# Optimization experiments

Hardware: AMD Instinct MI355X
Metric: run time of the kernel (lower is better)

Reference implementation:

```python
import jax, jax.numpy as jnp
import numpy as np

D, DFFN, H, P, L = 256, 1024, 8, 4, 4
B, LQ = 32, 300
LENS = [2048, 1024, 512, 256]
STARTS = [0, 2048, 3072, 3584]
S = sum(LENS)


def setup_inputs() -> dict:
    key = jax.random.key(0)
    ks = iter(jax.random.split(key, 64))
    def W(shape, s=0.02):
        return jax.random.normal(next(ks), shape, jnp.float32) * s
    inp = {}
    inp['tgt'] = W((B, LQ, D), 1.0)
    inp['query_pos'] = W((B, LQ, D), 1.0)
    centers = jax.random.uniform(next(ks), (B, LQ, L))
    widths = 0.05 + 0.2 * jax.random.uniform(next(ks), (B, LQ, L))
    inp['reference_points'] = jnp.stack([centers, widths], -1)  # (B,Lq,L,2) = (center,width)
    inp['src'] = W((B, S, D), 1.0)
    inp['temporal_lengths'] = np.array(LENS, np.int64)
    inp['level_start_index'] = np.array(STARTS, np.int64)
    for n, shape in [('sa_qw', (D, D)), ('sa_kw', (D, D)), ('sa_vw', (D, D)), ('sa_ow', (D, D)), ('ff1_w', (D, DFFN)), ('ff2_w', (DFFN, D))]:
        inp[n] = W(shape)
    for n, sz in [('sa_qb', D), ('sa_kb', D), ('sa_vb', D), ('sa_ob', D), ('ff1_b', DFFN), ('ff2_b', D)]:
        inp[n] = jnp.zeros((sz,), jnp.float32)
    for pre in ['ca', 'se']:
        inp[pre + '_off_w'] = W((D, H * L * P))
        inp[pre + '_off_b'] = jnp.zeros((H * L * P,), jnp.float32)
        inp[pre + '_attn_w'] = W((D, H * L * P))
        inp[pre + '_attn_b'] = jnp.zeros((H * L * P,), jnp.float32)
        inp[pre + '_val_w'] = W((D, D))
        inp[pre + '_val_b'] = jnp.zeros((D,), jnp.float32)
        inp[pre + '_out_w'] = W((D, D))
        inp[pre + '_out_b'] = jnp.zeros((D,), jnp.float32)
    for n in ['ln1', 'lnse', 'ln2', 'ln3']:
        inp[n + '_g'] = jnp.ones((D,), jnp.float32)
        inp[n + '_b'] = jnp.zeros((D,), jnp.float32)
    return inp


def _ln(x, g, b, eps=1e-5):
    m = jnp.mean(x, -1, keepdims=True)
    v = jnp.mean((x - m) ** 2, -1, keepdims=True)
    return (x - m) * jax.lax.rsqrt(v + eps) * g + b


def _mha(q, k, v, qw, qb, kw, kb, vw, vb, ow, ob):
    b, lq, d = q.shape
    dh = d // H
    qh = (q @ qw + qb).reshape(b, lq, H, dh).transpose(0, 2, 1, 3)
    kh = (k @ kw + kb).reshape(b, -1, H, dh).transpose(0, 2, 1, 3)
    vh = (v @ vw + vb).reshape(b, -1, H, dh).transpose(0, 2, 1, 3)
    scores = jnp.einsum('bhqd,bhkd->bhqk', qh, kh) * (dh ** -0.5)
    attn = jax.nn.softmax(scores, -1)
    out = jnp.einsum('bhqk,bhkd->bhqd', attn, vh).transpose(0, 2, 1, 3).reshape(b, lq, d)
    return out @ ow + ob


def _deform(q, ref, src, lens, starts, vw, vb, offw, offb, aw, ab, ow, ob, boundary):
    b, lq, d = q.shape
    dh = d // H
    value = (src @ vw + vb).reshape(b, -1, H, dh)  # (B,S,H,Dh)
    off = (q @ offw + offb).reshape(b, lq, H, L, P)
    attn = jax.nn.softmax((q @ aw + ab).reshape(b, lq, H, L * P), -1).reshape(b, lq, H, L, P)
    center = ref[..., 0][:, :, None, :, None]  # (B,Lq,1,L,1)
    width = ref[..., 1][:, :, None, :, None]
    if boundary:
        # half the points anchored at segment start, half at segment end
        sign = jnp.where(jnp.arange(P) < P // 2, -0.5, 0.5)
        anchor = center + sign * width
    else:
        anchor = center
    loc = anchor + off / P * width * 0.5  # normalized sampling locations (B,Lq,H,L,P)
    out = jnp.zeros((b, lq, H, dh), value.dtype)
    for l in range(L):
        T = int(lens[l]); s0 = int(starts[l])
        v = value[:, s0:s0 + T].transpose(0, 2, 1, 3)  # (B,H,T,Dh)
        x = loc[:, :, :, l, :] * T - 0.5  # align_corners=False grid
        x0 = jnp.floor(x)
        w = x - x0
        i0 = x0.astype(jnp.int32)
        i1 = i0 + 1
        m0 = ((i0 >= 0) & (i0 < T)).astype(v.dtype)
        m1 = ((i1 >= 0) & (i1 < T)).astype(v.dtype)
        i0c = jnp.clip(i0, 0, T - 1)
        i1c = jnp.clip(i1, 0, T - 1)
        def gather(idx):
            idxh = idx.transpose(0, 2, 1, 3).reshape(b, H, lq * P, 1)
            g = jnp.take_along_axis(v, jnp.broadcast_to(idxh, (b, H, lq * P, dh)), axis=2)
            return g.reshape(b, H, lq, P, dh).transpose(0, 2, 1, 3, 4)  # (B,Lq,H,P,Dh)
        samp = gather(i0c) * ((1 - w) * m0)[..., None] + gather(i1c) * (w * m1)[..., None]
        out = out + jnp.einsum('bqhp,bqhpd->bqhd', attn[:, :, :, l, :], samp)
    return out.reshape(b, lq, d) @ ow + ob


def reference(tgt, query_pos, reference_points, src, temporal_lengths, level_start_index,
              sa_qw, sa_qb, sa_kw, sa_kb, sa_vw, sa_vb, sa_ow, sa_ob,
              ca_off_w, ca_off_b, ca_attn_w, ca_attn_b, ca_val_w, ca_val_b, ca_out_w, ca_out_b,
              se_off_w, se_off_b, se_attn_w, se_attn_b, se_val_w, se_val_b, se_out_w, se_out_b,
              ff1_w, ff1_b, ff2_w, ff2_b,
              ln1_g, ln1_b, lnse_g, lnse_b, ln2_g, ln2_b, ln3_g, ln3_b):
    lens = np.asarray(temporal_lengths)
    starts = np.asarray(level_start_index)
    q = tgt + query_pos
    t2 = _mha(q, q, tgt, sa_qw, sa_qb, sa_kw, sa_kb, sa_vw, sa_vb, sa_ow, sa_ob)
    tgt = _ln(tgt + t2, ln2_g, ln2_b)
    t2 = _deform(tgt + query_pos, reference_points, src, lens, starts,
                 ca_val_w, ca_val_b, ca_off_w, ca_off_b, ca_attn_w, ca_attn_b, ca_out_w, ca_out_b, False)
    tgt = _ln(tgt + t2, ln1_g, ln1_b)
    t2 = _deform(tgt + query_pos, reference_points, src, lens, starts,
                 se_val_w, se_val_b, se_off_w, se_off_b, se_attn_w, se_attn_b, se_out_w, se_out_b, True)
    tgt = _ln(tgt + t2, lnse_g, lnse_b)
    t2 = jax.nn.relu(tgt @ ff1_w + ff1_b) @ ff2_w + ff2_b
    tgt = _ln(tgt + t2, ln3_g, ln3_b)
    return tgt
```

## Files before the change

### kernel.cpp

```cpp
#include <hip/hip_runtime.h>
#include <hip/hip_bf16.h>

namespace {

typedef unsigned short u16;
typedef unsigned int u32;

constexpr int D    = 256;
constexpr int H    = 8;
constexpr int DH   = 32;
constexpr int L    = 4;
constexpr int P    = 4;
constexpr int B    = 32;
constexpr int LQ   = 300;
constexpr int NQ   = B * LQ;
constexpr int S    = 3840;
constexpr int MS   = B * S;
constexpr int DFFN = 1024;

typedef __attribute__((ext_vector_type(8))) short bf16x8;
typedef __attribute__((ext_vector_type(4))) float f32x4;

__device__ inline u16 f2b(float x) {
  u32 u = __builtin_bit_cast(u32, x);
  u32 r = (u + 0x7FFFu + ((u >> 16) & 1u)) >> 16;
  return (u16)r;
}
__device__ inline u32 pk2(float a, float b) {
  return (u32)f2b(a) | ((u32)f2b(b) << 16);
}
__device__ inline void unpack2(u32 w, float& a, float& b) {
  a = __builtin_bit_cast(float, w << 16);
  b = __builtin_bit_cast(float, w & 0xffff0000u);
}

template<bool OUT_BF16, bool RELU>
__global__ __launch_bounds__(256) void gemm_sm(
    const u16* __restrict__ A, const u16* __restrict__ Bt,
    const float* __restrict__ bias, void* __restrict__ Cv,
    int M, int K, int N)
{
  constexpr int BM = 64, BN = 64, BK = 64, LDK = 72;
  __shared__ __align__(16) u16 sh[(BM + BN) * LDK];
  u16* As = sh;
  u16* Bs = sh + BM * LDK;
  const int tid  = threadIdx.x;
  const int lane = tid & 63;
  const int wid  = tid >> 6;
  const int wm = wid >> 1, wn = wid & 1;
  const int m0 = blockIdx.y * BM, n0 = blockIdx.x * BN;

  f32x4 acc[2][2] = {};
  uint4 ra[2], rb[2];
  const int NT = K / BK;
  const int srow = tid >> 3, sch = (tid & 7) * 8;

#pragma unroll
  for (int i = 0; i < 2; ++i) {
    const int row = srow + i * 32;
    ra[i] = *(const uint4*)(A  + (size_t)(m0 + row) * K + sch);
    rb[i] = *(const uint4*)(Bt + (size_t)(n0 + row) * K + sch);
  }

  for (int t = 0; t < NT; ++t) {
#pragma unroll
    for (int i = 0; i < 2; ++i) {
      const int row = srow + i * 32;
      *(uint4*)(&As[row * LDK + sch]) = ra[i];
      *(uint4*)(&Bs[row * LDK + sch]) = rb[i];
    }
    __syncthreads();
    if (t + 1 < NT) {
      const int k0 = (t + 1) * BK;
#pragma unroll
      for (int i = 0; i < 2; ++i) {
        const int row = srow + i * 32;
        ra[i] = *(const uint4*)(A  + (size_t)(m0 + row) * K + k0 + sch);
        rb[i] = *(const uint4*)(Bt + (size_t)(n0 + row) * K + k0 + sch);
      }
    }
#pragma unroll
    for (int kk = 0; kk < 2; ++kk) {
      const int krd = kk * 32 + (lane >> 4) * 8;
      bf16x8 af[2], bf[2];
#pragma unroll
      for (int m = 0; m < 2; ++m)
        af[m] = *(const bf16x8*)(&As[(wm * 32 + (lane & 15) + 16 * m) * LDK + krd]);
#pragma unroll
      for (int n = 0; n < 2; ++n)
        bf[n] = *(const bf16x8*)(&Bs[(wn * 32 + (lane & 15) + 16 * n) * LDK + krd]);
#pragma unroll
      for (int m = 0; m < 2; ++m)
#pragma unroll
        for (int n = 0; n < 2; ++n)
          acc[m][n] = __builtin_amdgcn_mfma_f32_16x16x32_bf16(af[m], bf[n], acc[m][n], 0, 0, 0);
    }
    __syncthreads();
  }

  const int cr = (lane >> 4) * 4;
  const int cc = lane & 15;
  if constexpr (OUT_BF16) {
    u16* stg = sh;
#pragma unroll
    for (int n = 0; n < 2; ++n) {
      const int lc = wn * 32 + n * 16 + cc;
      const float bv = bias[n0 + lc];
#pragma unroll
      for (int m = 0; m < 2; ++m) {
        const int lr0 = wm * 32 + m * 16 + cr;
#pragma unroll
        for (int r = 0; r < 4; ++r) {
          float x = acc[m][n][r] + bv;
          if (RELU) x = fmaxf(x, 0.f);
          stg[(lr0 + r) * LDK + lc] = f2b(x);
        }
      }
    }
    __syncthreads();
    u16* Cb = (u16*)Cv;
#pragma unroll
    for (int i = 0; i < 2; ++i) {
      const int c = tid + 256 * i;
      const int row = c >> 3, ch = c & 7;
      *(uint4*)(Cb + (size_t)(m0 + row) * N + n0 + ch * 8) =
          *(const uint4*)(&stg[row * LDK + ch * 8]);
    }
  } else {
#pragma unroll
    for (int n = 0; n < 2; ++n) {
      const int gc = n0 + wn * 32 + n * 16 + cc;
      const float bv = bias[gc];
#pragma unroll
      for (int m = 0; m < 2; ++m) {
        const int gr0 = m0 + wm * 32 + m * 16 + cr;
#pragma unroll
        for (int r = 0; r < 4; ++r) {
          float x = acc[m][n][r] + bv;
          if (RELU) x = fmaxf(x, 0.f);
          ((float*)Cv)[(size_t)(gr0 + r) * N + gc] = x;
        }
      }
    }
  }
}

__global__ __launch_bounds__(256) void gemm_qkv(
    const u16* __restrict__ qbuf, const u16* __restrict__ tgtb,
    const u16* __restrict__ saqk_t, const u16* __restrict__ sav_t,
    const float* __restrict__ qkb, const float* __restrict__ vbias,
    u16* __restrict__ qkbuf, u16* __restrict__ vh)
{
  constexpr int K = 256, BK = 64, LDK = 72;
  __shared__ __align__(16) u16 sh[128 * LDK];
  u16* As = sh;
  u16* Bs = sh + 64 * LDK;
  const bool isv = blockIdx.x >= 8;
  const u16* A  = isv ? tgtb : qbuf;
  const u16* Bt = isv ? sav_t : saqk_t;
  const float* bias = isv ? vbias : qkb;
  u16* C = isv ? vh : qkbuf;
  const int N = isv ? 256 : 512;
  const int n0 = (isv ? (int)blockIdx.x - 8 : (int)blockIdx.x) * 64;
  const int m0 = blockIdx.y * 64;

  const int tid  = threadIdx.x;
  const int lane = tid & 63;
  const int wid  = tid >> 6;
  const int wm = wid >> 1, wn = wid & 1;

  f32x4 acc[2][2] = {};
  uint4 ra[2], rb[2];
  const int srow = tid >> 3, sch = (tid & 7) * 8;

#pragma unroll
  for (int i = 0; i < 2; ++i) {
    const int row = srow + i * 32;
    ra[i] = *(const uint4*)(A  + (size_t)(m0 + row) * K + sch);
    rb[i] = *(const uint4*)(Bt + (size_t)(n0 + row) * K + sch);
  }
  for (int t = 0; t < 4; ++t) {
#pragma unroll
    for (int i = 0; i < 2; ++i) {
      const int row = srow + i * 32;
      *(uint4*)(&As[row * LDK + sch]) = ra[i];
      *(uint4*)(&Bs[row * LDK + sch]) = rb[i];
    }
    __syncthreads();
    if (t + 1 < 4) {
      const int k0 = (t + 1) * BK;
#pragma unroll
      for (int i = 0; i < 2; ++i) {
        const int row = srow + i * 32;
        ra[i] = *(const uint4*)(A  + (size_t)(m0 + row) * K + k0 + sch);
        rb[i] = *(const uint4*)(Bt + (size_t)(n0 + row) * K + k0 + sch);
      }
    }
#pragma unroll
    for (int kk = 0; kk < 2; ++kk) {
      const int krd = kk * 32 + (lane >> 4) * 8;
      bf16x8 af[2], bf[2];
#pragma unroll
      for (int m = 0; m < 2; ++m)
        af[m] = *(const bf16x8*)(&As[(wm * 32 + (lane & 15) + 16 * m) * LDK + krd]);
#pragma unroll
      for (int n = 0; n < 2; ++n)
        bf[n] = *(const bf16x8*)(&Bs[(wn * 32 + (lane & 15) + 16 * n) * LDK + krd]);
#pragma unroll
      for (int m = 0; m < 2; ++m)
#pragma unroll
        for (int n = 0; n < 2; ++n)
          acc[m][n] = __builtin_amdgcn_mfma_f32_16x16x32_bf16(af[m], bf[n], acc[m][n], 0, 0, 0);
    }
    __syncthreads();
  }

  const int cr = (lane >> 4) * 4;
  const int cc = lane & 15;
  u16* stg = sh;
#pragma unroll
  for (int n = 0; n < 2; ++n) {
    const int lc = wn * 32 + n * 16 + cc;
    const float bv = bias[n0 + lc];
#pragma unroll
    for (int m = 0; m < 2; ++m) {
      const int lr0 = wm * 32 + m * 16 + cr;
#pragma unroll
      for (int r = 0; r < 4; ++r)
        stg[(lr0 + r) * LDK + lc] = f2b(acc[m][n][r] + bv);
    }
  }
  __syncthreads();
#pragma unroll
  for (int i = 0; i < 2; ++i) {
    const int c = tid + 256 * i;
    const int row = c >> 3, ch = c & 7;
    *(uint4*)(C + (size_t)(m0 + row) * N + n0 + ch * 8) =
        *(const uint4*)(&stg[row * LDK + ch * 8]);
  }
}

__global__ __launch_bounds__(512) void gemm_val4(
    const float* __restrict__ A, const u16* __restrict__ Bt2,
    const float* __restrict__ bias2, u16* __restrict__ Vca, u16* __restrict__ Vse)
{
  __shared__ __align__(16) char shraw[33792];
  char* Asw = shraw;
  const int tid  = threadIdx.x;
  const int lane = tid & 63;
  const int w    = tid >> 6;
  const int nh   = blockIdx.x & 1;
  const int m0   = (blockIdx.x >> 1) * 64;
  u16* dst = nh ? Vse : Vca;
  const u16* Bt = Bt2 + nh * 256 * 256;
  const float* bias = bias2 + nh * 256;

#pragma unroll
  for (int i = 0; i < 4; ++i) {
    const int idx = tid + 512 * i;
    const int row = idx >> 5, ch = idx & 31;
    const float* ap = A + (size_t)(m0 + row) * 256 + ch * 8;
    const float4 f0 = *(const float4*)(ap);
    const float4 f1 = *(const float4*)(ap + 4);
    uint4 pk;
    pk.x = pk2(f0.x, f0.y); pk.y = pk2(f0.z, f0.w);
    pk.z = pk2(f1.x, f1.y); pk.w = pk2(f1.z, f1.w);
    *(uint4*)(Asw + row * 512 + ((ch * 16) ^ ((row & 7) << 4))) = pk;
  }
  __syncthreads();

  f32x4 acc[4][2] = {};
  const u16* bb = Bt + (size_t)(w * 32 + (lane & 15)) * 256 + (lane >> 4) * 8;
  bf16x8 bcur[2], bnxt[2];
#pragma unroll
  for (int n = 0; n < 2; ++n) bcur[n] = *(const bf16x8*)(bb + n * 4096);

#pragma unroll
  for (int kk = 0; kk < 8; ++kk) {
    bf16x8 af[4];
    const int kb = kk * 64 + (lane >> 4) * 16;
#pragma unroll
    for (int m = 0; m < 4; ++m) {
      const int row = m * 16 + (lane & 15);
      af[m] = *(const bf16x8*)(Asw + row * 512 + (kb ^ ((row & 7) << 4)));
    }
    if (kk < 7) {
#pragma unroll
      for (int n = 0; n < 2; ++n)
        bnxt[n] = *(const bf16x8*)(bb + n * 4096 + (kk + 1) * 32);
    }
#pragma unroll
    for (int m = 0; m < 4; ++m)
#pragma unroll
      for (int n = 0; n < 2; ++n)
        acc[m][n] = __builtin_amdgcn_mfma_f32_16x16x32_bf16(af[m], bcur[n], acc[m][n], 0, 0, 0);
#pragma unroll
    for (int n = 0; n < 2; ++n) bcur[n] = bnxt[n];
  }
  __syncthreads();

  constexpr int STC = 264;
  u16* stg = (u16*)shraw;
  const int cr = (lane >> 4) * 4;
  const int cc = lane & 15;
#pragma unroll
  for (int n = 0; n < 2; ++n) {
    const int col = w * 32 + n * 16 + cc;
    const float bv = bias[col];
#pragma unroll
    for (int m = 0; m < 4; ++m) {
      const int r0 = m * 16 + cr;
#pragma unroll
      for (int r = 0; r < 4; ++r)
        stg[(r0 + r) * STC + col] = f2b(acc[m][n][r] + bv);
    }
  }
  __syncthreads();
#pragma unroll
  for (int i = 0; i < 4; ++i) {
    const int c = tid + 512 * i;
    const int row = c >> 5, ch = c & 31;
    *(uint4*)(dst + (size_t)(m0 + row) * 256 + ch * 8) =
        *(const uint4*)(&stg[row * STC + ch * 8]);
  }
}

template<int MODE>
__global__ __launch_bounds__(1024) void gemm_ln(
    const u16* __restrict__ A, const u16* __restrict__ Bt,
    const float* __restrict__ bias, const float* __restrict__ res,
    const float* __restrict__ g, const float* __restrict__ be,
    const float* __restrict__ qpos,
    float* __restrict__ fout, u16* __restrict__ bfout, int K)
{
  constexpr int BK = 64, LDK = 72;
  __shared__ __align__(16) float ftile[64 * 264];
  u16* As = (u16*)ftile;
  u16* Bs = As + 64 * LDK;
  const int tid  = threadIdx.x;
  const int lane = tid & 63;
  const int wid  = tid >> 6;
  const int wm = wid >> 2, wn = wid & 3;
  const int m0 = blockIdx.x * 64;

  f32x4 acc[4] = {};
  const int NT = K / BK;
  const bool am = tid < 512;
  const int arow = tid >> 3, ach = (tid & 7) * 8;

  uint4 ra = {};
  uint4 rb[2];
  if (am) ra = *(const uint4*)(A + (size_t)(m0 + arow) * K + ach);
#pragma unroll
  for (int i = 0; i < 2; ++i) {
    const int idx = tid + 1024 * i;
    const int brow = idx >> 3, bch = (idx & 7) * 8;
    rb[i] = *(const uint4*)(Bt + (size_t)brow * K + bch);
  }

  for (int t = 0; t < NT; ++t) {
    if (am) *(uint4*)(&As[arow * LDK + ach]) = ra;
#pragma unroll
    for (int i = 0; i < 2; ++i) {
      const int idx = tid + 1024 * i;
      const int brow = idx >> 3, bch = (idx & 7) * 8;
      *(uint4*)(&Bs[brow * LDK + bch]) = rb[i];
    }
    __syncthreads();
    if (t + 1 < NT) {
      const int k0 = (t + 1) * BK;
      if (am) ra = *(const uint4*)(A + (size_t)(m0 + arow) * K + k0 + ach);
#pragma unroll
      for (int i = 0; i < 2; ++i) {
        const int idx = tid + 1024 * i;
        const int brow = idx >> 3, bch = (idx & 7) * 8;
        rb[i] = *(const uint4*)(Bt + (size_t)brow * K + k0 + bch);
      }
    }
#pragma unroll
    for (int kk = 0; kk < 2; ++kk) {
      const int krd = kk * 32 + (lane >> 4) * 8;
      bf16x8 af, bf[4];
      af = *(const bf16x8*)(&As[(wm * 16 + (lane & 15)) * LDK + krd]);
#pragma unroll
      for (int n = 0; n < 4; ++n)
        bf[n] = *(const bf16x8*)(&Bs[(wn * 64 + n * 16 + (lane & 15)) * LDK + krd]);
#pragma unroll
      for (int n = 0; n < 4; ++n)
        acc[n] = __builtin_amdgcn_mfma_f32_16x16x32_bf16(af, bf[n], acc[n], 0, 0, 0);
    }
    __syncthreads();
  }

  const int cr = (lane >> 4) * 4;
  const int cc = lane & 15;
#pragma unroll
  for (int n = 0; n < 4; ++n) {
    const int col = wn * 64 + n * 16 + cc;
    const float bv = bias[col];
#pragma unroll
    for (int r = 0; r < 4; ++r)
      ftile[(wm * 16 + cr + r) * 264 + col] = acc[n][r] + bv;
  }
  __syncthreads();

  const int row = tid >> 4, s16 = tid & 15;
  const size_t grow = (size_t)(m0 + row) * 256;
  float vv[16];
  float sum = 0.f;
#pragma unroll
  for (int j = 0; j < 4; ++j) {
    const int col = s16 * 4 + j * 64;
    const float4 fv = *(const float4*)(&ftile[row * 264 + col]);
    const float4 rv = *(const float4*)(res + grow + col);
    vv[j * 4 + 0] = fv.x + rv.x; vv[j * 4 + 1] = fv.y + rv.y;
    vv[j * 4 + 2] = fv.z + rv.z; vv[j * 4 + 3] = fv.w + rv.w;
    sum += vv[j * 4 + 0] + vv[j * 4 + 1] + vv[j * 4 + 2] + vv[j * 4 + 3];
  }
  sum += __shfl_xor(sum, 1, 64);
  sum += __shfl_xor(sum, 2, 64);
  sum += __shfl_xor(sum, 4, 64);
  sum += __shfl_xor(sum, 8, 64);
  const float mean = sum * (1.f / 256.f);
  float sq = 0.f;
#pragma unroll
  for (int k = 0; k < 16; ++k) { const float d = vv[k] - mean; sq += d * d; }
  sq += __shfl_xor(sq, 1, 64);
  sq += __shfl_xor(sq, 2, 64);
  sq += __shfl_xor(sq, 4, 64);
  sq += __shfl_xor(sq, 8, 64);
  const float rstd = rsqrtf(sq * (1.f / 256.f) + 1e-5f);

#pragma unroll
  for (int j = 0; j < 4; ++j) {
    const int col = s16 * 4 + j * 64;
    const float4 gv = *(const float4*)(g + col);
    const float4 bv = *(const float4*)(be + col);
    float4 y;
    y.x = (vv[j * 4 + 0] - mean) * rstd * gv.x + bv.x;
    y.y = (vv[j * 4 + 1] - mean) * rstd * gv.y + bv.y;
    y.z = (vv[j * 4 + 2] - mean) * rstd * gv.z + bv.z;
    y.w = (vv[j * 4 + 3] - mean) * rstd * gv.w + bv.w;
    *(float4*)(fout + grow + col) = y;
    if constexpr (MODE == 0) {
      const float4 qv = *(const float4*)(qpos + grow + col);
      uint2 pk;
      pk.x = pk2(y.x + qv.x, y.y + qv.y);
      pk.y = pk2(y.z + qv.z, y.w + qv.w);
      *(uint2*)(bfout + grow + col) = pk;
    } else if constexpr (MODE == 1) {
      uint2 pk;
      pk.x = pk2(y.x, y.y);
      pk.y = pk2(y.z, y.w);
      *(uint2*)(bfout + grow + col) = pk;
    }
  }
}

struct WSpec { const float* w; u16* wt; int K, N, blk0; };
struct WPack { WSpec s[14]; };

struct PrepArgs {
  const float *ca_off_b, *ca_attn_b, *se_off_b, *se_attn_b;
  const float *sa_qb, *sa_kb, *ca_val_b, *se_val_b;
  float *bias4, *qkb, *valb;
  const float *tgt, *qpos;
  u16 *tgtb, *qbuf;
  int n4, nwt;
};

__global__ __launch_bounds__(256) void prep_all(WPack p, PrepArgs a) {
  __shared__ float tile[32][33];
  const int b = blockIdx.x;
  if (b < a.nwt) {
    int i = 0;
#pragma unroll
    for (int j = 1; j < 14; ++j) if (b >= p.s[j].blk0) i = j;
    const float* w = p.s[i].w;
    u16* wt = p.s[i].wt;
    const int K = p.s[i].K, N = p.s[i].N;
    const int lb = b - p.s[i].blk0;
    const int ntN = N >> 5;
    const int tk = lb / ntN, tn = lb - tk * ntN;
    const int r = threadIdx.x >> 5, c = threadIdx.x & 31;
#pragma unroll
    for (int j = 0; j < 4; ++j)
      tile[r + j * 8][c] = w[(size_t)(tk * 32 + r + j * 8) * N + tn * 32 + c];
    __syncthreads();
#pragma unroll
    for (int j = 0; j < 4; ++j)
      wt[(size_t)(tn * 32 + r + j * 8) * K + tk * 32 + c] = f2b(tile[c][r + j * 8]);
  } else if (b == a.nwt) {
#pragma unroll
    for (int u = 0; u < 2; ++u) {
      const int t = threadIdx.x + 256 * u;
      a.bias4[t] = t < 128 ? a.ca_off_b[t] : t < 256 ? a.ca_attn_b[t - 128]
                 : t < 384 ? a.se_off_b[t - 256] : a.se_attn_b[t - 384];
      a.qkb[t]  = t < 256 ? a.sa_qb[t] : a.sa_kb[t - 256];
      a.valb[t] = t < 256 ? a.ca_val_b[t] : a.se_val_b[t - 256];
    }
  } else {
    const int i = (b - a.nwt - 1) * 256 + threadIdx.x;
    if (i < a.n4) {
      const float4 t = ((const float4*)a.tgt)[i];
      const float4 q = ((const float4*)a.qpos)[i];
      uint2 x, y;
      x.x = pk2(t.x, t.y); x.y = pk2(t.z, t.w);
      y.x = pk2(t.x + q.x, t.y + q.y); y.y = pk2(t.z + q.z, t.w + q.w);
      ((uint2*)a.tgtb)[i] = x;
      ((uint2*)a.qbuf)[i] = y;
    }
  }
}

__global__ __launch_bounds__(512) void mha_v2(
    const u16* __restrict__ qk, const u16* __restrict__ vh,
    u16* __restrict__ out)
{
  __shared__ __align__(16) float Ks[8 * 300 * 4];
  __shared__ __align__(16) float Vs[8 * 300 * 4];
  const int bh  = blockIdx.x & 255;
  const int seg = blockIdx.x >> 8;
  const int b = bh >> 3, h = bh & 7;
  const u16* kbase = qk + (size_t)b * LQ * 512 + 256 + h * DH;
  const u16* vbase = vh + (size_t)b * LQ * D + h * DH;
  for (int e = threadIdx.x; e < 300 * 8; e += 512) {
    const int r = e >> 3, j = e & 7;
    float4 f;
    const uint2 kv = *(const uint2*)(kbase + (size_t)r * 512 + j * 4);
    unpack2(kv.x, f.x, f.y);
    unpack2(kv.y, f.z, f.w);
    *(float4*)(&Ks[(j * 300 + r) * 4]) = f;
    const uint2 vv = *(const uint2*)(vbase + (size_t)r * D + j * 4);
    unpack2(vv.x, f.x, f.y);
    unpack2(vv.y, f.z, f.w);
    *(float4*)(&Vs[(j * 300 + r) * 4]) = f;
  }
  __syncthreads();

  const int lane = threadIdx.x & 63;
  const int lq = (threadIdx.x >> 6) * 16 + (lane >> 2);
  const int kc = lane & 3;
  const int q = seg * 128 + lq;
  if (q >= LQ) return;

  const u16* qrow = qk + (size_t)(b * LQ + q) * 512 + h * DH;
  float qv[DH];
#pragma unroll
  for (int c4 = 0; c4 < 4; ++c4) {
    const uint4 u = *(const uint4*)(qrow + c4 * 8);
    unpack2(u.x, qv[c4 * 8 + 0], qv[c4 * 8 + 1]);
    unpack2(u.y, qv[c4 * 8 + 2], qv[c4 * 8 + 3]);
    unpack2(u.z, qv[c4 * 8 + 4], qv[c4 * 8 + 5]);
    unpack2(u.w, qv[c4 * 8 + 6], qv[c4 * 8 + 7]);
  }
#pragma unroll
  for (int d = 0; d < DH; ++d) qv[d] *= 0.17677669529663689f;

  float o[DH] = {};
  float ssum = 0.f;
  const float* kp = &Ks[kc * 75 * 4];
  const float* vp = &Vs[kc * 75 * 4];
  for (int i = 0; i < 75; ++i) {
    float s = 0.f;
#pragma unroll
    for (int j = 0; j < 8; ++j) {
      const float4 kf = *(const float4*)(kp + i * 4 + j * 1200);
      s += qv[j * 4 + 0] * kf.x + qv[j * 4 + 1] * kf.y
         + qv[j * 4 + 2] * kf.z + qv[j * 4 + 3] * kf.w;
    }
    const float p = __expf(s);
    ssum += p;
#pragma unroll
    for (int j = 0; j < 8; ++j) {
      const float4 vf = *(const float4*)(vp + i * 4 + j * 1200);
      o[j * 4 + 0] += p * vf.x; o[j * 4 + 1] += p * vf.y;
      o[j * 4 + 2] += p * vf.z; o[j * 4 + 3] += p * vf.w;
    }
  }

  ssum += __shfl_xor(ssum, 1, 64);
  ssum += __shfl_xor(ssum, 2, 64);
#pragma unroll
  for (int d = 0; d < DH; ++d) {
    o[d] += __shfl_xor(o[d], 1, 64);
    o[d] += __shfl_xor(o[d], 2, 64);
  }
  const float inv = 1.f / ssum;

  u16* orow = out + (size_t)(b * LQ + q) * D + h * DH;
#pragma unroll
  for (int c = 0; c < 4; ++c) {
    if (kc == c) {
      uint4 w;
      w.x = pk2(o[c * 8 + 0] * inv, o[c * 8 + 1] * inv);
      w.y = pk2(o[c * 8 + 2] * inv, o[c * 8 + 3] * inv);
      w.z = pk2(o[c * 8 + 4] * inv, o[c * 8 + 5] * inv);
      w.w = pk2(o[c * 8 + 6] * inv, o[c * 8 + 7] * inv);
      *(uint4*)(orow + c * 8) = w;
    }
  }
}

template<bool BOUNDARY>
__global__ __launch_bounds__(512) void deform_v2(
    const float* __restrict__ oa, const float* __restrict__ ref,
    const u16* __restrict__ value, u16* __restrict__ out)
{
  __shared__ __align__(16) uint4 owt[4][128];
  const int unit = threadIdx.x >> 7;
  const int bq = blockIdx.x * 4 + unit;
  const int b = bq / LQ;
  const int t = threadIdx.x & 127;
  const int h = t >> 4;
  const int l = (t >> 2) & 3;
  const int p = t & 3;

  const float off   = oa[(size_t)bq * 256 + t];
  const float logit = oa[(size_t)bq * 256 + 128 + t];
  const float center = ref[(size_t)bq * 8 + l * 2 + 0];
  const float width  = ref[(size_t)bq * 8 + l * 2 + 1];

  const float e = __expf(logit);
  float ssum = e;
  ssum += __shfl_xor(ssum, 1, 64);
  ssum += __shfl_xor(ssum, 2, 64);
  ssum += __shfl_xor(ssum, 4, 64);
  ssum += __shfl_xor(ssum, 8, 64);
  const float wa = e / ssum;

  const int T  = 2048 >> l;
  const int s0 = 4096 - (4096 >> l);
  float anchor = center;
  if (BOUNDARY) anchor += (p < 2 ? -0.5f : 0.5f) * width;
  const float loc = anchor + off * width * 0.125f;
  const float x = loc * (float)T - 0.5f;
  const float x0 = floorf(x);
  const float w = x - x0;
  const int i0 = (int)x0;
  const int i1 = i0 + 1;
  const float w0 = (i0 >= 0 && i0 < T) ? wa * (1.f - w) : 0.f;
  const float w1 = (i1 >= 0 && i1 < T) ? wa * w : 0.f;
  const int i0c = min(max(i0, 0), T - 1);
  const int i1c = min(max(i1, 0), T - 1);
  uint4 pack;
  pack.x = (u32)((s0 + i0c) * (D * 2) + h * (DH * 2));
  pack.y = __builtin_bit_cast(u32, w0);
  pack.z = (u32)((s0 + i1c) * (D * 2) + h * (DH * 2));
  pack.w = __builtin_bit_cast(u32, w1);
  owt[unit][t] = pack;
  __syncthreads();

  const int g  = t >> 4;
  const int ln = t & 15;
  const char* vb = (const char*)(value + (size_t)b * S * D) + ln * 4;
  float o0 = 0.f, o1 = 0.f;
#pragma unroll
  for (int j = 0; j < 16; ++j) {
    const uint4 ow = owt[unit][g * 16 + j];
    const u32 v0 = *(const u32*)(vb + ow.x);
    const u32 v1 = *(const u32*)(vb + ow.z);
    const float wt0 = __builtin_bit_cast(float, ow.y);
    const float wt1 = __builtin_bit_cast(float, ow.w);
    float a, c;
    unpack2(v0, a, c); o0 += wt0 * a; o1 += wt0 * c;
    unpack2(v1, a, c); o0 += wt1 * a; o1 += wt1 * c;
  }
  const u32 res = pk2(o0, o1);
  *(u32*)(out + (size_t)bq * D + g * DH + ln * 2) = res;
}

}

extern "C" void kernel_launch(void* const* d_in, const int* in_sizes, int n_in,
                              void* d_out, int out_size, void* d_ws, size_t ws_size,
                              hipStream_t stream)
{
  const float* tgt   = (const float*)d_in[0];
  const float* qpos  = (const float*)d_in[1];
  const float* ref   = (const float*)d_in[2];
  const float* src   = (const float*)d_in[3];
  const float* sa_qw = (const float*)d_in[6];
  const float* sa_kw = (const float*)d_in[7];
  const float* sa_vw = (const float*)d_in[8];
  const float* sa_ow = (const float*)d_in[9];
  const float* ff1_w = (const float*)d_in[10];
  const float* ff2_w = (const float*)d_in[11];
  const float* sa_qb = (const float*)d_in[12];
  const float* sa_kb = (const float*)d_in[13];
  const float* sa_vb = (const float*)d_in[14];
  const float* sa_ob = (const float*)d_in[15];
  const float* ff1_b = (const float*)d_in[16];
  const float* ff2_b = (const float*)d_in[17];
  const float* ca_off_w  = (const float*)d_in[18];
  const float* ca_off_b  = (const float*)d_in[19];
  const float* ca_attn_w = (const float*)d_in[20];
  const float* ca_attn_b = (const float*)d_in[21];
  const float* ca_val_w  = (const float*)d_in[22];
  const float* ca_val_b  = (const float*)d_in[23];
  const float* ca_out_w  = (const float*)d_in[24];
  const float* ca_out_b  = (const float*)d_in[25];
  const float* se_off_w  = (const float*)d_in[26];
  const float* se_off_b  = (const float*)d_in[27];
  const float* se_attn_w = (const float*)d_in[28];
  const float* se_attn_b = (const float*)d_in[29];
  const float* se_val_w  = (const float*)d_in[30];
  const float* se_val_b  = (const float*)d_in[31];
  const float* se_out_w  = (const float*)d_in[32];
  const float* se_out_b  = (const float*)d_in[33];
  const float* ln1_g  = (const float*)d_in[34];
  const float* ln1_b  = (const float*)d_in[35];
  const float* lnse_g = (const float*)d_in[36];
  const float* lnse_b = (const float*)d_in[37];
  const float* ln2_g  = (const float*)d_in[38];
  const float* ln2_b  = (const float*)d_in[39];
  const float* ln3_g  = (const float*)d_in[40];
  const float* ln3_b  = (const float*)d_in[41];

  const size_t ND = (size_t)NQ * D;
  const size_t MD = (size_t)MS * D;

  char* base = (char*)d_ws;
  size_t off = 0;
  auto alloc = [&](size_t bytes) -> void* {
    void* p = base + off;
    off += (bytes + 255) & ~(size_t)255;
    return p;
  };
  u16*  Vca  = (u16*)alloc(MD * 2);
  u16*  Vse  = (u16*)alloc(MD * 2);
  u16*  qkbuf = (u16*)alloc((size_t)NQ * 512 * 2);
  u16*  vh   = (u16*)alloc(ND * 2);
  u16*  qbuf = (u16*)alloc(ND * 2);
  u16*  smpb = (u16*)alloc(ND * 2);
  u16*  tgtb = (u16*)alloc(ND * 2);
  u16*  curb = (u16*)alloc(ND * 2);
  float* cur = (float*)alloc(ND * 4);
  float* oabuf = (float*)alloc((size_t)NQ * 256 * 4);
  float* bias4 = (float*)alloc(512 * 4);
  float* qkb   = (float*)alloc(512 * 4);
  float* valb  = (float*)alloc(512 * 4);

  u16* ffh = Vca;

  WPack pk;
  int wi = 0, blk = 0;
  auto addw = [&](const float* w, int K, int N) -> u16* {
    u16* wt = (u16*)alloc((size_t)K * N * 2);
    pk.s[wi].w = w; pk.s[wi].wt = wt; pk.s[wi].K = K; pk.s[wi].N = N; pk.s[wi].blk0 = blk;
    blk += (K / 32) * (N / 32);
    ++wi;
    return wt;
  };
  u16* saq_t = addw(sa_qw, D, D);
  u16* sak_t = addw(sa_kw, D, D);        (void)sak_t;
  u16* sav_t = addw(sa_vw, D, D);
  u16* sao_t = addw(sa_ow, D, D);
  u16* ff1_t = addw(ff1_w, D, DFFN);
  u16* ff2_t = addw(ff2_w, DFFN, D);
  u16* caoff_t = addw(ca_off_w, D, 128);
  u16* caatt_t = addw(ca_attn_w, D, 128);  (void)caatt_t;
  u16* seoff_t = addw(se_off_w, D, 128);
  u16* seatt_t = addw(se_attn_w, D, 128);  (void)seatt_t;
  u16* caval_t = addw(ca_val_w, D, D);
  u16* seval_t = addw(se_val_w, D, D);     (void)seval_t;
  u16* caout_t = addw(ca_out_w, D, D);
  u16* seout_t = addw(se_out_w, D, D);

  const int n4 = (int)(ND / 4);

  PrepArgs pa;
  pa.ca_off_b = ca_off_b; pa.ca_attn_b = ca_attn_b;
  pa.se_off_b = se_off_b; pa.se_attn_b = se_attn_b;
  pa.sa_qb = sa_qb; pa.sa_kb = sa_kb; pa.ca_val_b = ca_val_b; pa.se_val_b = se_val_b;
  pa.bias4 = bias4; pa.qkb = qkb; pa.valb = valb;
  pa.tgt = tgt; pa.qpos = qpos; pa.tgtb = tgtb; pa.qbuf = qbuf;
  pa.n4 = n4; pa.nwt = blk;
  prep_all<<<blk + 1 + 2400, 256, 0, stream>>>(pk, pa);

  gemm_val4<<<(MS / 64) * 2, 512, 0, stream>>>(src, caval_t, valb, Vca, Vse);

  gemm_qkv<<<dim3(12, 150), 256, 0, stream>>>(qbuf, tgtb, saq_t, sav_t, qkb, sa_vb, qkbuf, vh);
  mha_v2<<<B * H * 3, 512, 0, stream>>>(qkbuf, vh, smpb);
  gemm_ln<0><<<NQ / 64, 1024, 0, stream>>>(smpb, sao_t, sa_ob, tgt, ln2_g, ln2_b, qpos, cur, qbuf, D);

  gemm_sm<false, false><<<dim3(4, 150), 256, 0, stream>>>(qbuf, caoff_t, bias4, oabuf, NQ, D, 256);
  deform_v2<false><<<NQ / 4, 512, 0, stream>>>(oabuf, ref, Vca, smpb);
  gemm_ln<0><<<NQ / 64, 1024, 0, stream>>>(smpb, caout_t, ca_out_b, cur, ln1_g, ln1_b, qpos, cur, qbuf, D);

  gemm_sm<false, false><<<dim3(4, 150), 256, 0, stream>>>(qbuf, seoff_t, bias4 + 256, oabuf, NQ, D, 256);
  deform_v2<true><<<NQ / 4, 512, 0, stream>>>(oabuf, ref, Vse, smpb);
  gemm_ln<1><<<NQ / 64, 1024, 0, stream>>>(smpb, seout_t, se_out_b, cur, lnse_g, lnse_b, nullptr, cur, curb, D);

  gemm_sm<true,  true ><<<dim3(16, 150), 256, 0, stream>>>(curb, ff1_t, ff1_b, ffh, NQ, D, DFFN);
  gemm_ln<2><<<NQ / 64, 1024, 0, stream>>>(ffh, ff2_t, ff2_b, cur, ln3_g, ln3_b, nullptr, (float*)d_out, nullptr, DFFN);
}
```

Before: 474.0 us.

## Merge QKV and value GEMMs into one launch, shrink LN-GEMM tiles, widen deform gathers

Three separate changes. First, the self-attention QKV projection and the src value projection now run as one launch, using 128-wide N tiles for QKV, which removes a launch and lets the two GEMMs share the machine. Second, gemm_ln moves from 64-row tiles with 1024 threads to 16-row tiles with 256 threads, giving 600 blocks instead of 150 for better CU occupancy, at the cost of reloading the full weight matrix per block. Third, the deformable gather loads 16-byte vectors per sample instead of 4-byte words and reduces across lanes with shuffles, cutting the number of load instructions in exchange for shuffle work.

```diff
diff --git a/kernel.cpp b/kernel.cpp
--- a/kernel.cpp
+++ b/kernel.cpp
@@ -9,8 +9,6 @@
 constexpr int D    = 256;
 constexpr int H    = 8;
 constexpr int DH   = 32;
-constexpr int L    = 4;
-constexpr int P    = 4;
 constexpr int B    = 32;
 constexpr int LQ   = 300;
 constexpr int NQ   = B * LQ;
@@ -145,246 +143,245 @@
   }
 }
 
-__global__ __launch_bounds__(256) void gemm_qkv(
+__global__ __launch_bounds__(512) void gemm_big(
+    const float* __restrict__ src, const u16* __restrict__ valw_t,
+    const float* __restrict__ valb, u16* __restrict__ Vca, u16* __restrict__ Vse,
     const u16* __restrict__ qbuf, const u16* __restrict__ tgtb,
     const u16* __restrict__ saqk_t, const u16* __restrict__ sav_t,
     const float* __restrict__ qkb, const float* __restrict__ vbias,
     u16* __restrict__ qkbuf, u16* __restrict__ vh)
 {
-  constexpr int K = 256, BK = 64, LDK = 72;
-  __shared__ __align__(16) u16 sh[128 * LDK];
-  u16* As = sh;
-  u16* Bs = sh + 64 * LDK;
-  const bool isv = blockIdx.x >= 8;
-  const u16* A  = isv ? tgtb : qbuf;
-  const u16* Bt = isv ? sav_t : saqk_t;
-  const float* bias = isv ? vbias : qkb;
-  u16* C = isv ? vh : qkbuf;
-  const int N = isv ? 256 : 512;
-  const int n0 = (isv ? (int)blockIdx.x - 8 : (int)blockIdx.x) * 64;
-  const int m0 = blockIdx.y * 64;
-
+  __shared__ __align__(16) char shraw[33792];
   const int tid  = threadIdx.x;
   const int lane = tid & 63;
-  const int wid  = tid >> 6;
-  const int wm = wid >> 1, wn = wid & 1;
-
-  f32x4 acc[2][2] = {};
-  uint4 ra[2], rb[2];
-  const int srow = tid >> 3, sch = (tid & 7) * 8;
-
-#pragma unroll
-  for (int i = 0; i < 2; ++i) {
-    const int row = srow + i * 32;
-    ra[i] = *(const uint4*)(A  + (size_t)(m0 + row) * K + sch);
-    rb[i] = *(const uint4*)(Bt + (size_t)(n0 + row) * K + sch);
-  }
-  for (int t = 0; t < 4; ++t) {
+  const int bx = blockIdx.x;
+
+  if (bx < 900) {
+    constexpr int K = 256, LDK = 72;
+    u16* As = (u16*)shraw;
+    u16* Bs = As + 64 * LDK;
+    const int nt = bx % 6;
+    const int m0 = (bx / 6) * 64;
+    const bool isv = nt >= 4;
+    const int nrel = isv ? nt - 4 : nt;
+    const u16* A  = isv ? tgtb : qbuf;
+    const u16* Bt = (isv ? sav_t : saqk_t) + (size_t)nrel * 128 * 256;
+    const float* bias = (isv ? vbias : qkb) + nrel * 128;
+    u16* C = isv ? vh : qkbuf;
+    const int N = isv ? 256 : 512;
+    const int n0 = nrel * 128;
+
+    const int wid = tid >> 6;
+    const int wm = wid >> 2, wn = wid & 3;
+
+    f32x4 acc[2][2] = {};
+    const int arow = tid >> 3, ach = (tid & 7) * 8;
+    uint4 ra, rb[2];
+    ra = *(const uint4*)(A + (size_t)(m0 + arow) * K + ach);
 #pragma unroll
     for (int i = 0; i < 2; ++i) {
-      const int row = srow + i * 32;
-      *(uint4*)(&As[row * LDK + sch]) = ra[i];
-      *(uint4*)(&Bs[row * LDK + sch]) = rb[i];
-    }
-    __syncthreads();
-    if (t + 1 < 4) {
-      const int k0 = (t + 1) * BK;
+      const int idx = tid + 512 * i;
+      rb[i] = *(const uint4*)(Bt + (size_t)(idx >> 3) * K + (idx & 7) * 8);
+    }
+    for (int t = 0; t < 4; ++t) {
+      *(uint4*)(&As[arow * LDK + ach]) = ra;
 #pragma unroll
       for (int i = 0; i < 2; ++i) {
-        const int row = srow + i * 32;
-        ra[i] = *(const uint4*)(A  + (size_t)(m0 + row) * K + k0 + sch);
-        rb[i] = *(const uint4*)(Bt + (size_t)(n0 + row) * K + k0 + sch);
-      }
-    }
-#pragma unroll
-    for (int kk = 0; kk < 2; ++kk) {
-      const int krd = kk * 32 + (lane >> 4) * 8;
-      bf16x8 af[2], bf[2];
-#pragma unroll
-      for (int m = 0; m < 2; ++m)
-        af[m] = *(const bf16x8*)(&As[(wm * 32 + (lane & 15) + 16 * m) * LDK + krd]);
-#pragma unroll
-      for (int n = 0; n < 2; ++n)
-        bf[n] = *(const bf16x8*)(&Bs[(wn * 32 + (lane & 15) + 16 * n) * LDK + krd]);
-#pragma unroll
-      for (int m = 0; m < 2; ++m)
+        const int idx = tid + 512 * i;
+        *(uint4*)(&Bs[(idx >> 3) * LDK + (idx & 7) * 8]) = rb[i];
+      }
+      __syncthreads();
+      if (t + 1 < 4) {
+        const int k0 = (t + 1) * 64;
+        ra = *(const uint4*)(A + (size_t)(m0 + arow) * K + k0 + ach);
+#pragma unroll
+        for (int i = 0; i < 2; ++i) {
+          const int idx = tid + 512 * i;
+          rb[i] = *(const uint4*)(Bt + (size_t)(idx >> 3) * K + k0 + (idx & 7) * 8);
+        }
+      }
+#pragma unroll
+      for (int kk = 0; kk < 2; ++kk) {
+        const int krd = kk * 32 + (lane >> 4) * 8;
+        bf16x8 af[2], bf[2];
+#pragma unroll
+        for (int m = 0; m < 2; ++m)
+          af[m] = *(const bf16x8*)(&As[(wm * 32 + m * 16 + (lane & 15)) * LDK + krd]);
 #pragma unroll
         for (int n = 0; n < 2; ++n)
-          acc[m][n] = __builtin_amdgcn_mfma_f32_16x16x32_bf16(af[m], bf[n], acc[m][n], 0, 0, 0);
-    }
-    __syncthreads();
-  }
-
-  const int cr = (lane >> 4) * 4;
-  const int cc = lane & 15;
-  u16* stg = sh;
-#pragma unroll
-  for (int n = 0; n < 2; ++n) {
-    const int lc = wn * 32 + n * 16 + cc;
-    const float bv = bias[n0 + lc];
-#pragma unroll
-    for (int m = 0; m < 2; ++m) {
-      const int lr0 = wm * 32 + m * 16 + cr;
-#pragma unroll
-      for (int r = 0; r < 4; ++r)
-        stg[(lr0 + r) * LDK + lc] = f2b(acc[m][n][r] + bv);
-    }
-  }
-  __syncthreads();
-#pragma unroll
-  for (int i = 0; i < 2; ++i) {
-    const int c = tid + 256 * i;
-    const int row = c >> 3, ch = c & 7;
-    *(uint4*)(C + (size_t)(m0 + row) * N + n0 + ch * 8) =
-        *(const uint4*)(&stg[row * LDK + ch * 8]);
-  }
-}
-
-__global__ __launch_bounds__(512) void gemm_val4(
-    const float* __restrict__ A, const u16* __restrict__ Bt2,
-    const float* __restrict__ bias2, u16* __restrict__ Vca, u16* __restrict__ Vse)
-{
-  __shared__ __align__(16) char shraw[33792];
-  char* Asw = shraw;
-  const int tid  = threadIdx.x;
-  const int lane = tid & 63;
-  const int w    = tid >> 6;
-  const int nh   = blockIdx.x & 1;
-  const int m0   = (blockIdx.x >> 1) * 64;
-  u16* dst = nh ? Vse : Vca;
-  const u16* Bt = Bt2 + nh * 256 * 256;
-  const float* bias = bias2 + nh * 256;
-
-#pragma unroll
-  for (int i = 0; i < 4; ++i) {
-    const int idx = tid + 512 * i;
-    const int row = idx >> 5, ch = idx & 31;
-    const float* ap = A + (size_t)(m0 + row) * 256 + ch * 8;
-    const float4 f0 = *(const float4*)(ap);
-    const float4 f1 = *(const float4*)(ap + 4);
-    uint4 pk;
-    pk.x = pk2(f0.x, f0.y); pk.y = pk2(f0.z, f0.w);
-    pk.z = pk2(f1.x, f1.y); pk.w = pk2(f1.z, f1.w);
-    *(uint4*)(Asw + row * 512 + ((ch * 16) ^ ((row & 7) << 4))) = pk;
-  }
-  __syncthreads();
-
-  f32x4 acc[4][2] = {};
-  const u16* bb = Bt + (size_t)(w * 32 + (lane & 15)) * 256 + (lane >> 4) * 8;
-  bf16x8 bcur[2], bnxt[2];
-#pragma unroll
-  for (int n = 0; n < 2; ++n) bcur[n] = *(const bf16x8*)(bb + n * 4096);
-
-#pragma unroll
-  for (int kk = 0; kk < 8; ++kk) {
-    bf16x8 af[4];
-    const int kb = kk * 64 + (lane >> 4) * 16;
-#pragma unroll
-    for (int m = 0; m < 4; ++m) {
-      const int row = m * 16 + (lane & 15);
-      af[m] = *(const bf16x8*)(Asw + row * 512 + (kb ^ ((row & 7) << 4)));
-    }
-    if (kk < 7) {
-#pragma unroll
-      for (int n = 0; n < 2; ++n)
-        bnxt[n] = *(const bf16x8*)(bb + n * 4096 + (kk + 1) * 32);
-    }
-#pragma unroll
-    for (int m = 0; m < 4; ++m)
-#pragma unroll
-      for (int n = 0; n < 2; ++n)
-        acc[m][n] = __builtin_amdgcn_mfma_f32_16x16x32_bf16(af[m], bcur[n], acc[m][n], 0, 0, 0);
-#pragma unroll
-    for (int n = 0; n < 2; ++n) bcur[n] = bnxt[n];
-  }
-  __syncthreads();
-
-  constexpr int STC = 264;
-  u16* stg = (u16*)shraw;
-  const int cr = (lane >> 4) * 4;
-  const int cc = lane & 15;
-#pragma unroll
-  for (int n = 0; n < 2; ++n) {
-    const int col = w * 32 + n * 16 + cc;
-    const float bv = bias[col];
-#pragma unroll
-    for (int m = 0; m < 4; ++m) {
-      const int r0 = m * 16 + cr;
-#pragma unroll
-      for (int r = 0; r < 4; ++r)
-        stg[(r0 + r) * STC + col] = f2b(acc[m][n][r] + bv);
-    }
-  }
-  __syncthreads();
-#pragma unroll
-  for (int i = 0; i < 4; ++i) {
-    const int c = tid + 512 * i;
-    const int row = c >> 5, ch = c & 31;
-    *(uint4*)(dst + (size_t)(m0 + row) * 256 + ch * 8) =
-        *(const uint4*)(&stg[row * STC + ch * 8]);
+          bf[n] = *(const bf16x8*)(&Bs[(wn * 32 + n * 16 + (lane & 15)) * LDK + krd]);
+#pragma unroll
+        for (int m = 0; m < 2; ++m)
+#pragma unroll
+          for (int n = 0; n < 2; ++n)
+            acc[m][n] = __builtin_amdgcn_mfma_f32_16x16x32_bf16(af[m], bf[n], acc[m][n], 0, 0, 0);
+      }
+      __syncthreads();
+    }
+    constexpr int STC = 136;
+    u16* stg = (u16*)shraw;
+    const int cr = (lane >> 4) * 4;
+    const int cc = lane & 15;
+#pragma unroll
+    for (int n = 0; n < 2; ++n) {
+      const int lc = wn * 32 + n * 16 + cc;
+      const float bv = bias[lc];
+#pragma unroll
+      for (int m = 0; m < 2; ++m) {
+        const int lr0 = wm * 32 + m * 16 + cr;
+#pragma unroll
+        for (int r = 0; r < 4; ++r)
+          stg[(lr0 + r) * STC + lc] = f2b(acc[m][n][r] + bv);
+      }
+    }
+    __syncthreads();
+#pragma unroll
+    for (int i = 0; i < 2; ++i) {
+      const int c = tid + 512 * i;
+      const int row = c >> 4, ch = c & 15;
+      *(uint4*)(C + (size_t)(m0 + row) * N + n0 + ch * 8) =
+          *(const uint4*)(&stg[row * STC + ch * 8]);
+    }
+    return;
+  }
+
+  {
+    const int vx = bx - 900;
+    char* Asw = shraw;
+    const int w    = tid >> 6;
+    const int nh   = vx & 1;
+    const int m0   = (vx >> 1) * 64;
+    u16* dst = nh ? Vse : Vca;
+    const u16* Bt = valw_t + nh * 256 * 256;
+    const float* bias = valb + nh * 256;
+
+#pragma unroll
+    for (int i = 0; i < 4; ++i) {
+      const int idx = tid + 512 * i;
+      const int row = idx >> 5, ch = idx & 31;
+      const float* ap = src + (size_t)(m0 + row) * 256 + ch * 8;
+      const float4 f0 = *(const float4*)(ap);
+      const float4 f1 = *(const float4*)(ap + 4);
+      uint4 pk;
+      pk.x = pk2(f0.x, f0.y); pk.y = pk2(f0.z, f0.w);
+      pk.z = pk2(f1.x, f1.y); pk.w = pk2(f1.z, f1.w);
+      *(uint4*)(Asw + row * 512 + ((ch * 16) ^ ((row & 7) << 4))) = pk;
+    }
+    __syncthreads();
+
+    f32x4 acc[4][2] = {};
+    const u16* bb = Bt + (size_t)(w * 32 + (lane & 15)) * 256 + (lane >> 4) * 8;
+    bf16x8 bcur[2], bnxt[2];
+#pragma unroll
+    for (int n = 0; n < 2; ++n) bcur[n] = *(const bf16x8*)(bb + n * 4096);
+
+#pragma unroll
+    for (int kk = 0; kk < 8; ++kk) {
+      bf16x8 af[4];
+      const int kb = kk * 64 + (lane >> 4) * 16;
+#pragma unroll
+      for (int m = 0; m < 4; ++m) {
+        const int row = m * 16 + (lane & 15);
+        af[m] = *(const bf16x8*)(Asw + row * 512 + (kb ^ ((row & 7) << 4)));
+      }
+      if (kk < 7) {
+#pragma unroll
+        for (int n = 0; n < 2; ++n)
+          bnxt[n] = *(const bf16x8*)(bb + n * 4096 + (kk + 1) * 32);
+      }
+#pragma unroll
+      for (int m = 0; m < 4; ++m)
+#pragma unroll
+        for (int n = 0; n < 2; ++n)
+          acc[m][n] = __builtin_amdgcn_mfma_f32_16x16x32_bf16(af[m], bcur[n], acc[m][n], 0, 0, 0);
+#pragma unroll
+      for (int n = 0; n < 2; ++n) bcur[n] = bnxt[n];
+    }
+    __syncthreads();
+
+    constexpr int STC = 264;
+    u16* stg = (u16*)shraw;
+    const int cr = (lane >> 4) * 4;
+    const int cc = lane & 15;
+#pragma unroll
+    for (int n = 0; n < 2; ++n) {
+      const int col = w * 32 + n * 16 + cc;
+      const float bv = bias[col];
+#pragma unroll
+      for (int m = 0; m < 4; ++m) {
+        const int r0 = m * 16 + cr;
+#pragma unroll
+        for (int r = 0; r < 4; ++r)
+          stg[(r0 + r) * STC + col] = f2b(acc[m][n][r] + bv);
+      }
+    }
+    __syncthreads();
+#pragma unroll
+    for (int i = 0; i < 4; ++i) {
+      const int c = tid + 512 * i;
+      const int row = c >> 5, ch = c & 31;
+      *(uint4*)(dst + (size_t)(m0 + row) * 256 + ch * 8) =
+          *(const uint4*)(&stg[row * STC + ch * 8]);
+    }
   }
 }
 
 template<int MODE>
-__global__ __launch_bounds__(1024) void gemm_ln(
+__global__ __launch_bounds__(256) void gemm_ln(
     const u16* __restrict__ A, const u16* __restrict__ Bt,
     const float* __restrict__ bias, const float* __restrict__ res,
     const float* __restrict__ g, const float* __restrict__ be,
     const float* __restrict__ qpos,
     float* __restrict__ fout, u16* __restrict__ bfout, int K)
 {
-  constexpr int BK = 64, LDK = 72;
-  __shared__ __align__(16) float ftile[64 * 264];
-  u16* As = (u16*)ftile;
-  u16* Bs = As + 64 * LDK;
+  constexpr int LDK = 72;
+  __shared__ __align__(16) char shraw[(16 + 256) * LDK * 2];
+  u16* As = (u16*)shraw;
+  u16* Bs = As + 16 * LDK;
+  float* ftile = (float*)shraw;
   const int tid  = threadIdx.x;
   const int lane = tid & 63;
   const int wid  = tid >> 6;
-  const int wm = wid >> 2, wn = wid & 3;
-  const int m0 = blockIdx.x * 64;
+  const int m0 = blockIdx.x * 16;
 
   f32x4 acc[4] = {};
-  const int NT = K / BK;
-  const bool am = tid < 512;
+  const int NT = K / 64;
   const int arow = tid >> 3, ach = (tid & 7) * 8;
 
   uint4 ra = {};
-  uint4 rb[2];
-  if (am) ra = *(const uint4*)(A + (size_t)(m0 + arow) * K + ach);
-#pragma unroll
-  for (int i = 0; i < 2; ++i) {
-    const int idx = tid + 1024 * i;
-    const int brow = idx >> 3, bch = (idx & 7) * 8;
-    rb[i] = *(const uint4*)(Bt + (size_t)brow * K + bch);
+  uint4 rb[8];
+  if (tid < 128) ra = *(const uint4*)(A + (size_t)(m0 + arow) * K + ach);
+#pragma unroll
+  for (int i = 0; i < 8; ++i) {
+    const int idx = tid + 256 * i;
+    rb[i] = *(const uint4*)(Bt + (size_t)(idx >> 3) * K + (idx & 7) * 8);
   }
 
   for (int t = 0; t < NT; ++t) {
-    if (am) *(uint4*)(&As[arow * LDK + ach]) = ra;
-#pragma unroll
-    for (int i = 0; i < 2; ++i) {
-      const int idx = tid + 1024 * i;
-      const int brow = idx >> 3, bch = (idx & 7) * 8;
-      *(uint4*)(&Bs[brow * LDK + bch]) = rb[i];
+    if (tid < 128) *(uint4*)(&As[arow * LDK + ach]) = ra;
+#pragma unroll
+    for (int i = 0; i < 8; ++i) {
+      const int idx = tid + 256 * i;
+      *(uint4*)(&Bs[(idx >> 3) * LDK + (idx & 7) * 8]) = rb[i];
     }
     __syncthreads();
     if (t + 1 < NT) {
-      const int k0 = (t + 1) * BK;
-      if (am) ra = *(const uint4*)(A + (size_t)(m0 + arow) * K + k0 + ach);
-#pragma unroll
-      for (int i = 0; i < 2; ++i) {
-        const int idx = tid + 1024 * i;
-        const int brow = idx >> 3, bch = (idx & 7) * 8;
-        rb[i] = *(const uint4*)(Bt + (size_t)brow * K + k0 + bch);
+      const int k0 = (t + 1) * 64;
+      if (tid < 128) ra = *(const uint4*)(A + (size_t)(m0 + arow) * K + k0 + ach);
+#pragma unroll
+      for (int i = 0; i < 8; ++i) {
+        const int idx = tid + 256 * i;
+        rb[i] = *(const uint4*)(Bt + (size_t)(idx >> 3) * K + k0 + (idx & 7) * 8);
       }
     }
 #pragma unroll
     for (int kk = 0; kk < 2; ++kk) {
       const int krd = kk * 32 + (lane >> 4) * 8;
       bf16x8 af, bf[4];
-      af = *(const bf16x8*)(&As[(wm * 16 + (lane & 15)) * LDK + krd]);
+      af = *(const bf16x8*)(&As[(lane & 15) * LDK + krd]);
 #pragma unroll
       for (int n = 0; n < 4; ++n)
-        bf[n] = *(const bf16x8*)(&Bs[(wn * 64 + n * 16 + (lane & 15)) * LDK + krd]);
+        bf[n] = *(const bf16x8*)(&Bs[(wid * 64 + n * 16 + (lane & 15)) * LDK + krd]);
 #pragma unroll
       for (int n = 0; n < 4; ++n)
         acc[n] = __builtin_amdgcn_mfma_f32_16x16x32_bf16(af, bf[n], acc[n], 0, 0, 0);
@@ -396,11 +393,11 @@
   const int cc = lane & 15;
 #pragma unroll
   for (int n = 0; n < 4; ++n) {
-    const int col = wn * 64 + n * 16 + cc;
+    const int col = wid * 64 + n * 16 + cc;
     const float bv = bias[col];
 #pragma unroll
     for (int r = 0; r < 4; ++r)
-      ftile[(wm * 16 + cr + r) * 264 + col] = acc[n][r] + bv;
+      ftile[(cr + r) * 264 + col] = acc[n][r] + bv;
   }
   __syncthreads();
 
@@ -603,7 +600,7 @@
 }
 
 template<bool BOUNDARY>
-__global__ __launch_bounds__(512) void deform_v2(
+__global__ __launch_bounds__(512) void deform_v3(
     const float* __restrict__ oa, const float* __restrict__ ref,
     const u16* __restrict__ value, u16* __restrict__ out)
 {
@@ -653,21 +650,34 @@
 
   const int g  = t >> 4;
   const int ln = t & 15;
-  const char* vb = (const char*)(value + (size_t)b * S * D) + ln * 4;
-  float o0 = 0.f, o1 = 0.f;
-#pragma unroll
-  for (int j = 0; j < 16; ++j) {
-    const uint4 ow = owt[unit][g * 16 + j];
-    const u32 v0 = *(const u32*)(vb + ow.x);
-    const u32 v1 = *(const u32*)(vb + ow.z);
-    const float wt0 = __builtin_bit_cast(float, ow.y);
-    const float wt1 = __builtin_bit_cast(float, ow.w);
-    float a, c;
-    unpack2(v0, a, c); o0 += wt0 * a; o1 += wt0 * c;
-    unpack2(v1, a, c); o0 += wt1 * a; o1 += wt1 * c;
-  }
-  const u32 res = pk2(o0, o1);
-  *(u32*)(out + (size_t)bq * D + g * DH + ln * 2) = res;
+  const int qd = ln & 3;
+  const int ts = ln >> 2;
+  const char* vb = (const char*)(value + (size_t)b * S * D) + qd * 16;
+  float o[8] = {};
+#pragma unroll
+  for (int i = 0; i < 8; ++i) {
+    const int rowidx = i * 4 + ts;
+    const uint4 ow = owt[unit][g * 16 + (rowidx >> 1)];
+    const u32 boff = (rowidx & 1) ? ow.z : ow.x;
+    const float wt = __builtin_bit_cast(float, (rowidx & 1) ? ow.w : ow.y);
+    const uint4 v = *(const uint4*)(vb + boff);
+    float a0, a1;
+    unpack2(v.x, a0, a1); o[0] += wt * a0; o[1] += wt * a1;
+    unpack2(v.y, a0, a1); o[2] += wt * a0; o[3] += wt * a1;
+    unpack2(v.z, a0, a1); o[4] += wt * a0; o[5] += wt * a1;
+    unpack2(v.w, a0, a1); o[6] += wt * a0; o[7] += wt * a1;
+  }
+#pragma unroll
+  for (int d = 0; d < 8; ++d) {
+    o[d] += __shfl_xor(o[d], 4, 64);
+    o[d] += __shfl_xor(o[d], 8, 64);
+  }
+  if (ts == 0) {
+    uint4 wv;
+    wv.x = pk2(o[0], o[1]); wv.y = pk2(o[2], o[3]);
+    wv.z = pk2(o[4], o[5]); wv.w = pk2(o[6], o[7]);
+    *(uint4*)(out + (size_t)bq * D + g * DH + qd * 8) = wv;
+  }
 }
 
 }
@@ -778,20 +788,21 @@
   pa.n4 = n4; pa.nwt = blk;
   prep_all<<<blk + 1 + 2400, 256, 0, stream>>>(pk, pa);
 
-  gemm_val4<<<(MS / 64) * 2, 512, 0, stream>>>(src, caval_t, valb, Vca, Vse);
-
-  gemm_qkv<<<dim3(12, 150), 256, 0, stream>>>(qbuf, tgtb, saq_t, sav_t, qkb, sa_vb, qkbuf, vh);
+  gemm_big<<<900 + (MS / 64) * 2, 512, 0, stream>>>(
+      src, caval_t, valb, Vca, Vse,
+      qbuf, tgtb, saq_t, sav_t, qkb, sa_vb, qkbuf, vh);
+
   mha_v2<<<B * H * 3, 512, 0, stream>>>(qkbuf, vh, smpb);
-  gemm_ln<0><<<NQ / 64, 1024, 0, stream>>>(smpb, sao_t, sa_ob, tgt, ln2_g, ln2_b, qpos, cur, qbuf, D);
+  gemm_ln<0><<<NQ / 16, 256, 0, stream>>>(smpb, sao_t, sa_ob, tgt, ln2_g, ln2_b, qpos, cur, qbuf, D);
 
   gemm_sm<false, false><<<dim3(4, 150), 256, 0, stream>>>(qbuf, caoff_t, bias4, oabuf, NQ, D, 256);
-  deform_v2<false><<<NQ / 4, 512, 0, stream>>>(oabuf, ref, Vca, smpb);
-  gemm_ln<0><<<NQ / 64, 1024, 0, stream>>>(smpb, caout_t, ca_out_b, cur, ln1_g, ln1_b, qpos, cur, qbuf, D);
+  deform_v3<false><<<NQ / 4, 512, 0, stream>>>(oabuf, ref, Vca, smpb);
+  gemm_ln<0><<<NQ / 16, 256, 0, stream>>>(smpb, caout_t, ca_out_b, cur, ln1_g, ln1_b, qpos, cur, qbuf, D);
 
   gemm_sm<false, false><<<dim3(4, 150), 256, 0, stream>>>(qbuf, seoff_t, bias4 + 256, oabuf, NQ, D, 256);
-  deform_v2<true><<<NQ / 4, 512, 0, stream>>>(oabuf, ref, Vse, smpb);
-  gemm_ln<1><<<NQ / 64, 1024, 0, stream>>>(smpb, seout_t, se_out_b, cur, lnse_g, lnse_b, nullptr, cur, curb, D);
+  deform_v3<true><<<NQ / 4, 512, 0, stream>>>(oabuf, ref, Vse, smpb);
+  gemm_ln<1><<<NQ / 16, 256, 0, stream>>>(smpb, seout_t, se_out_b, cur, lnse_g, lnse_b, nullptr, cur, curb, D);
 
   gemm_sm<true,  true ><<<dim3(16, 150), 256, 0, stream>>>(curb, ff1_t, ff1_b, ffh, NQ, D, DFFN);
-  gemm_ln<2><<<NQ / 64, 1024, 0, stream>>>(ffh, ff2_t, ff2_b, cur, ln3_g, ln3_b, nullptr, (float*)d_out, nullptr, DFFN);
-}
+  gemm_ln<2><<<NQ / 16, 256, 0, stream>>>(ffh, ff2_t, ff2_b, cur, ln3_g, ln3_b, nullptr, (float*)d_out, nullptr, DFFN);
+}
```

Measured after the change: 570.7 us. +20.4%, slower.
